# Optimization experiments

Measured on AMD Instinct MI355X. Metric: run time of the kernel, lower is better.

Reference implementation:

```python
import jax, jax.numpy as jnp
import numpy as np

TEMPERATURE = 0.1
NUM_CLASSES = 100


def setup_inputs() -> dict:
    key = jax.random.key(0)
    k1, k2 = jax.random.split(key)
    embeddings = jax.random.normal(k1, (8192, 128), dtype=jnp.float32)
    labels = jax.random.randint(k2, (8192,), 0, NUM_CLASSES, dtype=jnp.int64)
    return {"embeddings": embeddings, "labels": labels}


def reference(embeddings, labels):
    # L2-normalize rows (eps matches torch.nn.functional.normalize clamp)
    norm = jnp.maximum(jnp.linalg.norm(embeddings, axis=1, keepdims=True), 1e-12)
    e = embeddings / norm
    sim = jnp.matmul(e, e.T) / TEMPERATURE  # [N, N]
    n = sim.shape[0]
    eye = jnp.eye(n, dtype=bool)
    # positives: same label, excluding self
    pos = (labels[None, :] == labels[:, None]) & ~eye
    # The per-row torch loop computes soft-target cross-entropy over all
    # non-diagonal entries: row_loss_i = -sum_{j in pos(i)} log_softmax(sim[i, j!=i])_j.
    # log_softmax is permutation-invariant, so concatenation order is irrelevant.
    neg_inf = jnp.finfo(sim.dtype).min
    masked = jnp.where(eye, neg_inf, sim)
    logz = jax.nn.logsumexp(masked, axis=1, keepdims=True)  # [N, 1]
    logp = sim - logz  # [N, N]
    row_loss = -jnp.sum(jnp.where(pos, logp, 0.0), axis=1)  # rows with no positives contribute 0
    return jnp.sum(row_loss) / n
```

## Files before the change

### kernel.cpp

```cpp
#include <hip/hip_runtime.h>


#define N 8192
#define D 128
#define JSPLIT 32
#define IBLK 256
#define K2E 14.4269504088896340736f

typedef __bf16 bf16x8 __attribute__((ext_vector_type(8)));
typedef float f32x4 __attribute__((ext_vector_type(4)));

#define EBF_OFF  0
#define CNT_OFF  2097152
#define Z_OFF    2097664
#define S_OFF    2130432
#define ZERO_SZ  (512 + 32768 + 32768)

__device__ __forceinline__ unsigned short f32_to_bf16_rne(float f) {
    unsigned int u = __float_as_uint(f);
    u += 0x7fffu + ((u >> 16) & 1u);
    return (unsigned short)(u >> 16);
}


__global__ __launch_bounds__(256) void prep_kernel(
        const float* __restrict__ emb, const int* __restrict__ labels,
        unsigned char* __restrict__ ebf, int* __restrict__ cnt) {
    const int wave = threadIdx.x >> 6;
    const int lane = threadIdx.x & 63;
    const int row  = blockIdx.x * 4 + wave;

    const float2 v = *(const float2*)(emb + (size_t)row * D + lane * 2);
    float ss = v.x * v.x + v.y * v.y;
    #pragma unroll
    for (int off = 32; off; off >>= 1) ss += __shfl_xor(ss, off);
    const float inv = 1.0f / fmaxf(sqrtf(ss), 1e-12f);

    const int grp = row >> 4, col = row & 15;
    const int c = lane >> 4, q = (lane >> 2) & 3, j2 = lane & 3;
    unsigned int packed = (unsigned int)f32_to_bf16_rne(v.x * inv) |
                          ((unsigned int)f32_to_bf16_rne(v.y * inv) << 16);
    *(unsigned int*)(ebf + grp * 4096 + c * 1024 + q * 256 + col * 16 + j2 * 4) = packed;

    if (lane == 0) atomicAdd(&cnt[labels[row]], 1);
}

__global__ __launch_bounds__(256) void zsum_kernel(
        const unsigned char* __restrict__ ebf, const int* __restrict__ labels,
        float* __restrict__ z, float* __restrict__ s) {
    const int t    = threadIdx.x;
    const int w    = t >> 6;
    const int lane = t & 63;
    const int q    = lane >> 4;
    const int col  = lane & 15;
    const int iw   = blockIdx.x * IBLK + w * 64;
    const int jb   = blockIdx.y * (N / JSPLIT);

    bf16x8 a[4][4];
    int labi[4][4];
    #pragma unroll
    for (int g = 0; g < 4; ++g) {
        const unsigned char* ag = ebf + (size_t)(iw / 16 + g) * 4096 + lane * 16;
        #pragma unroll
        for (int c = 0; c < 4; ++c) a[g][c] = *(const bf16x8*)(ag + c * 1024);
        const int4 li = *(const int4*)(labels + iw + g * 16 + q * 4);
        labi[g][0] = li.x; labi[g][1] = li.y; labi[g][2] = li.z; labi[g][3] = li.w;
    }

    float zacc[4][4] = {{0.f,0.f,0.f,0.f},{0.f,0.f,0.f,0.f},
                        {0.f,0.f,0.f,0.f},{0.f,0.f,0.f,0.f}};
    float pacc[4][4] = {{0.f,0.f,0.f,0.f},{0.f,0.f,0.f,0.f},
                        {0.f,0.f,0.f,0.f},{0.f,0.f,0.f,0.f}};

    #pragma unroll 4
    for (int jt = 0; jt < (N / JSPLIT) / 16; ++jt) {
        const int js = jb + jt * 16;
        const unsigned char* bg = ebf + (size_t)(js / 16) * 4096 + lane * 16;
        bf16x8 b[4];
        #pragma unroll
        for (int c = 0; c < 4; ++c) b[c] = *(const bf16x8*)(bg + c * 1024);
        const int labj = labels[js + col];

        #pragma unroll
        for (int g = 0; g < 4; ++g) {
            f32x4 acc = {0.f, 0.f, 0.f, 0.f};
            #pragma unroll
            for (int c = 0; c < 4; ++c)
                acc = __builtin_amdgcn_mfma_f32_16x16x32_bf16(a[g][c], b[c], acc, 0, 0, 0);
            if (js == iw + g * 16) {
                #pragma unroll
                for (int r = 0; r < 4; ++r) {
                    const bool self = (col == q * 4 + r);
                    zacc[g][r] += self ? 0.0f : exp2f(fmaf(acc[r], K2E, -K2E));
                    pacc[g][r] += (!self && labj == labi[g][r]) ? acc[r] : 0.0f;
                }
            } else {
                #pragma unroll
                for (int r = 0; r < 4; ++r) {
                    zacc[g][r] += exp2f(fmaf(acc[r], K2E, -K2E));
                    pacc[g][r] += (labj == labi[g][r]) ? acc[r] : 0.0f;
                }
            }
        }
    }

    #pragma unroll
    for (int g = 0; g < 4; ++g)
        #pragma unroll
        for (int r = 0; r < 4; ++r) {
            float zv = zacc[g][r], pv = pacc[g][r];
            zv += __shfl_xor(zv, 1); pv += __shfl_xor(pv, 1);
            zv += __shfl_xor(zv, 2); pv += __shfl_xor(pv, 2);
            zv += __shfl_xor(zv, 4); pv += __shfl_xor(pv, 4);
            zv += __shfl_xor(zv, 8); pv += __shfl_xor(pv, 8);
            if (col == 0) {
                const int row = iw + g * 16 + q * 4 + r;
                atomicAdd(&z[row], zv);
                atomicAdd(&s[row], pv);
            }
        }
}

__global__ __launch_bounds__(1024) void final_kernel(
        const int* __restrict__ labels, const int* __restrict__ cnt,
        const float* __restrict__ z, const float* __restrict__ s,
        float* __restrict__ out) {
    __shared__ float part[16];
    const int tid = threadIdx.x;
    float acc = 0.0f;
    #pragma unroll
    for (int k = 0; k < N / 1024; ++k) {
        const int row = k * 1024 + tid;
        const int P = cnt[labels[row]] - 1;
        if (P > 0)
            acc += (float)P * (10.0f + logf(z[row])) - 10.0f * s[row];
    }
    #pragma unroll
    for (int off = 32; off; off >>= 1) acc += __shfl_xor(acc, off);
    if ((tid & 63) == 0) part[tid >> 6] = acc;
    __syncthreads();
    if (tid == 0) {
        float tot = 0.0f;
        #pragma unroll
        for (int w = 0; w < 16; ++w) tot += part[w];
        out[0] = tot * (1.0f / (float)N);
    }
}

extern "C" void kernel_launch(void* const* d_in, const int* in_sizes, int n_in,
                              void* d_out, int out_size, void* d_ws, size_t ws_size,
                              hipStream_t stream) {
    const float* emb  = (const float*)d_in[0];
    const int* labels = (const int*)d_in[1];
    float* out        = (float*)d_out;
    char* ws          = (char*)d_ws;

    unsigned char* ebf = (unsigned char*)(ws + EBF_OFF);
    int*   cnt         = (int*)(ws + CNT_OFF);
    float* z           = (float*)(ws + Z_OFF);
    float* s           = (float*)(ws + S_OFF);

    hipMemsetAsync(ws + CNT_OFF, 0, ZERO_SZ, stream);

    prep_kernel<<<N / 4, 256, 0, stream>>>(emb, labels, ebf, cnt);
    zsum_kernel<<<dim3(N / IBLK, JSPLIT), 256, 0, stream>>>(ebf, labels, z, s);
    final_kernel<<<1, 1024, 0, stream>>>(labels, cnt, z, s, out);
}
```

Baseline: 131.1 us.

## Compute positive-pair sum via per-class embedding sums instead of in the N² loop

Replaces the per-pair positive-logit accumulation inside the N×N MFMA loop with an algebraic identity: the sum over same-label pairs equals the sum over classes of ||class sum||² minus N for the self terms. A new ssum_kernel builds per-class normalized embedding sums in fp32, and the final kernel sums their squares. This drops the label loads, compares and second accumulator from the hot loop, which also adds register prefetching of the next B tile and uses the hardware exp2/log intrinsics. The cost is an extra kernel that scans all rows once per class, and positive similarities are now taken in fp32 rather than from bf16 MFMA output.

```diff
diff --git a/kernel.cpp b/kernel.cpp
--- a/kernel.cpp
+++ b/kernel.cpp
@@ -3,18 +3,23 @@
 
 #define N 8192
 #define D 128
+#define NCLS 100
 #define JSPLIT 32
 #define IBLK 256
+#define NJT ((N / JSPLIT) / 16)
+#define SCH 8
 #define K2E 14.4269504088896340736f
+#define LN2 0.69314718055994530942f
 
 typedef __bf16 bf16x8 __attribute__((ext_vector_type(8)));
 typedef float f32x4 __attribute__((ext_vector_type(4)));
 
-#define EBF_OFF  0
-#define CNT_OFF  2097152
-#define Z_OFF    2097664
-#define S_OFF    2130432
-#define ZERO_SZ  (512 + 32768 + 32768)
+#define EBF_OFF 0u
+#define INV_OFF 0x200000u
+#define CNT_OFF 0x208000u
+#define Z_OFF   0x208200u
+#define SP_OFF  0x210200u
+#define ZERO_SZ (512u + 32768u)
 
 __device__ __forceinline__ unsigned short f32_to_bf16_rne(float f) {
     unsigned int u = __float_as_uint(f);
@@ -25,7 +30,8 @@
 
 __global__ __launch_bounds__(256) void prep_kernel(
         const float* __restrict__ emb, const int* __restrict__ labels,
-        unsigned char* __restrict__ ebf, int* __restrict__ cnt) {
+        unsigned char* __restrict__ ebf, int* __restrict__ cnt,
+        float* __restrict__ invn) {
     const int wave = threadIdx.x >> 6;
     const int lane = threadIdx.x & 63;
     const int row  = blockIdx.x * 4 + wave;
@@ -42,12 +48,30 @@
                           ((unsigned int)f32_to_bf16_rne(v.y * inv) << 16);
     *(unsigned int*)(ebf + grp * 4096 + c * 1024 + q * 256 + col * 16 + j2 * 4) = packed;
 
-    if (lane == 0) atomicAdd(&cnt[labels[row]], 1);
+    if (lane == 0) {
+        invn[row] = inv;
+        atomicAdd(&cnt[labels[row]], 1);
+    }
+}
+
+__global__ __launch_bounds__(128) void ssum_kernel(
+        const float* __restrict__ emb, const int* __restrict__ labels,
+        const float* __restrict__ invn, float* __restrict__ spart) {
+    const int c  = blockIdx.x;
+    const int ch = blockIdx.y;
+    const int d  = threadIdx.x;
+    const int r0 = ch * (N / SCH);
+    float acc = 0.0f;
+    #pragma unroll 4
+    for (int r = r0; r < r0 + N / SCH; ++r) {
+        if (labels[r] == c)
+            acc += emb[(size_t)r * D + d] * invn[r];
+    }
+    spart[(ch * NCLS + c) * D + d] = acc;
 }
 
 __global__ __launch_bounds__(256) void zsum_kernel(
-        const unsigned char* __restrict__ ebf, const int* __restrict__ labels,
-        float* __restrict__ z, float* __restrict__ s) {
+        const unsigned char* __restrict__ ebf, float* __restrict__ z) {
     const int t    = threadIdx.x;
     const int w    = t >> 6;
     const int lane = t & 63;
@@ -57,73 +81,73 @@
     const int jb   = blockIdx.y * (N / JSPLIT);
 
     bf16x8 a[4][4];
-    int labi[4][4];
     #pragma unroll
     for (int g = 0; g < 4; ++g) {
         const unsigned char* ag = ebf + (size_t)(iw / 16 + g) * 4096 + lane * 16;
         #pragma unroll
         for (int c = 0; c < 4; ++c) a[g][c] = *(const bf16x8*)(ag + c * 1024);
-        const int4 li = *(const int4*)(labels + iw + g * 16 + q * 4);
-        labi[g][0] = li.x; labi[g][1] = li.y; labi[g][2] = li.z; labi[g][3] = li.w;
     }
 
     float zacc[4][4] = {{0.f,0.f,0.f,0.f},{0.f,0.f,0.f,0.f},
                         {0.f,0.f,0.f,0.f},{0.f,0.f,0.f,0.f}};
-    float pacc[4][4] = {{0.f,0.f,0.f,0.f},{0.f,0.f,0.f,0.f},
-                        {0.f,0.f,0.f,0.f},{0.f,0.f,0.f,0.f}};
-
-    #pragma unroll 4
-    for (int jt = 0; jt < (N / JSPLIT) / 16; ++jt) {
+
+    const unsigned char* bbase = ebf + (size_t)(jb / 16) * 4096 + lane * 16;
+
+    bf16x8 bc[4];
+    #pragma unroll
+    for (int c = 0; c < 4; ++c) bc[c] = *(const bf16x8*)(bbase + c * 1024);
+
+    #pragma unroll 2
+    for (int jt = 0; jt < NJT; ++jt) {
         const int js = jb + jt * 16;
-        const unsigned char* bg = ebf + (size_t)(js / 16) * 4096 + lane * 16;
-        bf16x8 b[4];
-        #pragma unroll
-        for (int c = 0; c < 4; ++c) b[c] = *(const bf16x8*)(bg + c * 1024);
-        const int labj = labels[js + col];
+
+        const int jn = (jt + 1 < NJT) ? jt + 1 : jt;
+        bf16x8 bn[4];
+        {
+            const unsigned char* bg = bbase + (size_t)jn * 4096;
+            #pragma unroll
+            for (int c = 0; c < 4; ++c) bn[c] = *(const bf16x8*)(bg + c * 1024);
+        }
 
         #pragma unroll
         for (int g = 0; g < 4; ++g) {
             f32x4 acc = {0.f, 0.f, 0.f, 0.f};
             #pragma unroll
             for (int c = 0; c < 4; ++c)
-                acc = __builtin_amdgcn_mfma_f32_16x16x32_bf16(a[g][c], b[c], acc, 0, 0, 0);
+                acc = __builtin_amdgcn_mfma_f32_16x16x32_bf16(a[g][c], bc[c], acc, 0, 0, 0);
             if (js == iw + g * 16) {
                 #pragma unroll
-                for (int r = 0; r < 4; ++r) {
-                    const bool self = (col == q * 4 + r);
-                    zacc[g][r] += self ? 0.0f : exp2f(fmaf(acc[r], K2E, -K2E));
-                    pacc[g][r] += (!self && labj == labi[g][r]) ? acc[r] : 0.0f;
-                }
+                for (int r = 0; r < 4; ++r)
+                    zacc[g][r] += (col == q * 4 + r) ? 0.0f
+                        : __builtin_amdgcn_exp2f(fmaf(acc[r], K2E, -K2E));
             } else {
                 #pragma unroll
-                for (int r = 0; r < 4; ++r) {
-                    zacc[g][r] += exp2f(fmaf(acc[r], K2E, -K2E));
-                    pacc[g][r] += (labj == labi[g][r]) ? acc[r] : 0.0f;
-                }
+                for (int r = 0; r < 4; ++r)
+                    zacc[g][r] += __builtin_amdgcn_exp2f(fmaf(acc[r], K2E, -K2E));
             }
         }
+
+        #pragma unroll
+        for (int c = 0; c < 4; ++c) bc[c] = bn[c];
     }
 
     #pragma unroll
     for (int g = 0; g < 4; ++g)
         #pragma unroll
         for (int r = 0; r < 4; ++r) {
-            float zv = zacc[g][r], pv = pacc[g][r];
-            zv += __shfl_xor(zv, 1); pv += __shfl_xor(pv, 1);
-            zv += __shfl_xor(zv, 2); pv += __shfl_xor(pv, 2);
-            zv += __shfl_xor(zv, 4); pv += __shfl_xor(pv, 4);
-            zv += __shfl_xor(zv, 8); pv += __shfl_xor(pv, 8);
-            if (col == 0) {
-                const int row = iw + g * 16 + q * 4 + r;
-                atomicAdd(&z[row], zv);
-                atomicAdd(&s[row], pv);
-            }
+            float zv = zacc[g][r];
+            zv += __shfl_xor(zv, 1);
+            zv += __shfl_xor(zv, 2);
+            zv += __shfl_xor(zv, 4);
+            zv += __shfl_xor(zv, 8);
+            if (col == 0)
+                atomicAdd(&z[iw + g * 16 + q * 4 + r], zv);
         }
 }
 
 __global__ __launch_bounds__(1024) void final_kernel(
         const int* __restrict__ labels, const int* __restrict__ cnt,
-        const float* __restrict__ z, const float* __restrict__ s,
+        const float* __restrict__ z, const float* __restrict__ spart,
         float* __restrict__ out) {
     __shared__ float part[16];
     const int tid = threadIdx.x;
@@ -133,7 +157,17 @@
         const int row = k * 1024 + tid;
         const int P = cnt[labels[row]] - 1;
         if (P > 0)
-            acc += (float)P * (10.0f + logf(z[row])) - 10.0f * s[row];
+            acc += (float)P * fmaf(LN2, __builtin_amdgcn_logf(z[row]), 10.0f);
+    }
+    #pragma unroll
+    for (int k = 0; k < (NCLS * D + 1023) / 1024; ++k) {
+        const int idx = k * 1024 + tid;
+        if (idx < NCLS * D) {
+            float sv = 0.0f;
+            #pragma unroll
+            for (int ch = 0; ch < SCH; ++ch) sv += spart[ch * (NCLS * D) + idx];
+            acc -= 10.0f * sv * sv;
+        }
     }
     #pragma unroll
     for (int off = 32; off; off >>= 1) acc += __shfl_xor(acc, off);
@@ -143,7 +177,7 @@
         float tot = 0.0f;
         #pragma unroll
         for (int w = 0; w < 16; ++w) tot += part[w];
-        out[0] = tot * (1.0f / (float)N);
+        out[0] = (tot + 10.0f * (float)N) * (1.0f / (float)N);
     }
 }
 
@@ -156,13 +190,15 @@
     char* ws          = (char*)d_ws;
 
     unsigned char* ebf = (unsigned char*)(ws + EBF_OFF);
+    float* invn        = (float*)(ws + INV_OFF);
     int*   cnt         = (int*)(ws + CNT_OFF);
     float* z           = (float*)(ws + Z_OFF);
-    float* s           = (float*)(ws + S_OFF);
+    float* spart       = (float*)(ws + SP_OFF);
 
     hipMemsetAsync(ws + CNT_OFF, 0, ZERO_SZ, stream);
 
-    prep_kernel<<<N / 4, 256, 0, stream>>>(emb, labels, ebf, cnt);
-    zsum_kernel<<<dim3(N / IBLK, JSPLIT), 256, 0, stream>>>(ebf, labels, z, s);
-    final_kernel<<<1, 1024, 0, stream>>>(labels, cnt, z, s, out);
-}
+    prep_kernel<<<N / 4, 256, 0, stream>>>(emb, labels, ebf, cnt, invn);
+    ssum_kernel<<<dim3(NCLS, SCH), 128, 0, stream>>>(emb, labels, invn, spart);
+    zsum_kernel<<<dim3(N / IBLK, JSPLIT), 256, 0, stream>>>(ebf, z);
+    final_kernel<<<1, 1024, 0, stream>>>(labels, cnt, z, spart, out);
+}
```

Measured after the change: 156.6 us. 19.4% more time.
